# Optimization experiments

Hardware: AMD Instinct MI355X
Metric: run time of the kernel (lower is better)

Reference implementation:

```python
import jax, jax.numpy as jnp
import numpy as np

RES_SCALE = 0.1
B, C, H, W = 16, 256, 96, 96


def conv3x3(x, w):
    # NCHW input, OIHW weight, SAME padding (padding=1 for k=3), no bias
    return jax.lax.conv_general_dilated(
        x, w, window_strides=(1, 1), padding="SAME",
        dimension_numbers=("NCHW", "OIHW", "NCHW"))


def setup_inputs() -> dict:
    key = jax.random.key(0)
    k1, k2, k3, k4 = jax.random.split(key, 4)
    fan = C * 9
    x = jax.random.normal(k1, (B, C, H, W), dtype=jnp.float32)
    conv2_w = jax.random.normal(k2, (C, C, 3, 3), dtype=jnp.float32) / np.sqrt(fan)
    conv3_w = jax.random.normal(k3, (C, C, 3, 3), dtype=jnp.float32) / np.sqrt(fan)
    prelu_w = jnp.full((1,), 0.25, dtype=jnp.float32)  # nn.PReLU default init
    # interleaved channel partition: P=0::3 (86), R=1::3 (85), T=2::3 (85)
    idx_p = jnp.arange(0, C, 3, dtype=jnp.int32)
    idx_r = jnp.arange(1, C, 3, dtype=jnp.int32)
    idx_t = jnp.arange(2, C, 3, dtype=jnp.int32)
    return {"x": x, "conv2_w": conv2_w, "conv3_w": conv3_w, "prelu_w": prelu_w,
            "idx_p": idx_p, "idx_r": idx_r, "idx_t": idx_t}


def reference(x, conv2_w, conv3_w, prelu_w, idx_p, idx_r, idx_t):
    # op2 = conv2(prune(x, skip_gate)) ; all-ones gate -> identity prune
    op2 = conv3x3(x, conv2_w)  # [B, C, H, W]
    # per-channel activation routing (gathers permute channel order to [P,R,T])
    gp = op2[:, idx_p]                                  # [B, 86, H, W]
    a = jnp.concatenate([
        jnp.where(gp >= 0, gp, prelu_w[0] * gp),        # PReLU (1 shared param)
        jax.nn.relu(op2[:, idx_r]),                     # [B, 85, H, W]
        jnp.tanh(op2[:, idx_t]),                        # [B, 85, H, W]
    ], axis=1)                                          # [B, C, H, W]
    # conv_tot branch: op3 = conv3(a)*res_scale + x * reshape(skip_conv_gate)
    # skip_conv_gate == ones here, so the skip scaling is identity
    op3 = conv3x3(a, conv3_w) * RES_SCALE + x
    return op3


if __name__ == "__main__":
    out = reference(**setup_inputs())
    print(out.shape, out.dtype)
```

## Files before the change

### kernel.cpp

```cpp
#include <hip/hip_runtime.h>
#include <math.h>


#define Bn 16
#define Cn 256
#define Hn 96
#define Wn 96
#define PH 98
#define PW 98
#define HW (Hn*Wn)

typedef __bf16 bf16x8 __attribute__((ext_vector_type(8)));
typedef float  f32x4  __attribute__((ext_vector_type(4)));

__device__ __forceinline__ unsigned short f2bf(float f) {
    unsigned int u = __float_as_uint(f);
    unsigned int r = (u + 0x7fffu + ((u >> 16) & 1u)) >> 16;
    return (unsigned short)r;
}

__device__ __forceinline__ void lds_load16(void* lds, const void* g) {
    auto gp = (const __attribute__((address_space(1))) char*)(unsigned long long)(uintptr_t)g;
    auto lp = (__attribute__((address_space(3))) char*)(unsigned int)(uintptr_t)lds;
    __builtin_amdgcn_global_load_lds(gp, lp, 16, 0, 0);
}

#define SB() __builtin_amdgcn_sched_barrier(0)
#define MEMFENCE() asm volatile("" ::: "memory")

__global__ __launch_bounds__(256)
void zero_border_k(unsigned short* __restrict__ t) {
    int idx = blockIdx.x * 256 + threadIdx.x;
    int oct = idx & 31;
    int rest = idx >> 5;
    int pidx = rest % 388;
    int b = rest / 388;
    int h, w;
    if (pidx < 98)       { h = 0;  w = pidx; }
    else if (pidx < 196) { h = 97; w = pidx - 98; }
    else if (pidx < 292) { h = pidx - 196 + 1; w = 0; }
    else                 { h = pidx - 292 + 1; w = 97; }
    size_t e = ((size_t)(b * PH + h) * PW + w) * 256 + oct * 8;
    *(uint4*)(t + e) = make_uint4(0u, 0u, 0u, 0u);
}

template<bool PERM>
__global__ __launch_bounds__(256)
void pack_w_k(const float* __restrict__ w, unsigned short* __restrict__ wp) {
    int idx = blockIdx.x * 256 + threadIdx.x;
    int ci_l = idx & 31;
    int c    = (idx >> 5) & 255;
    int v    = idx >> 13;
    int k9   = v % 9;
    int cc   = v / 9;
    int co;
    if (PERM) {
        co = (c < 86) ? c * 3 : (c < 171) ? (c - 86) * 3 + 1 : (c - 171) * 3 + 2;
    } else {
        co = c;
    }
    float val = w[((size_t)co * 256 + cc * 32 + ci_l) * 9 + k9];
    wp[idx] = f2bf(val);
}

__global__ __launch_bounds__(256)
void transform_x_k(const float* __restrict__ x, unsigned short* __restrict__ xp) {
    __shared__ float s[32 * 33];
    const int t = threadIdx.x;
    const int col0 = blockIdx.x * 32;
    const int row  = blockIdx.y;
    const int z = blockIdx.z;
    const int b = z >> 3;
    const int ci0 = (z & 7) * 32;

    #pragma unroll
    for (int i = 0; i < 4; ++i) {
        int ci = i * 8 + (t >> 5);
        int px = t & 31;
        s[ci * 33 + px] = x[((size_t)(b * Cn + ci0 + ci)) * HW + row * Wn + col0 + px];
    }
    __syncthreads();
    const int px = t >> 3;
    const int c4 = (t & 7) * 4;
    ushort4 o;
    o.x = f2bf(s[(c4 + 0) * 33 + px]);
    o.y = f2bf(s[(c4 + 1) * 33 + px]);
    o.z = f2bf(s[(c4 + 2) * 33 + px]);
    o.w = f2bf(s[(c4 + 3) * 33 + px]);
    size_t e = ((size_t)(b * PH + row + 1) * PW + (col0 + px + 1)) * 256 + ci0 + c4;
    *(ushort4*)(xp + e) = o;
}

template<int MODE>
__global__ __launch_bounds__(512) __attribute__((amdgpu_waves_per_eu(2, 2)))
void conv_k(const unsigned short* __restrict__ in_cl,
            const unsigned short* __restrict__ wp,
            const float* __restrict__ prelu_w,
            const float* __restrict__ xres,
            void* __restrict__ outp)
{
    __shared__ unsigned short s_x[2][2048 * 8];
    __shared__ unsigned short s_w[2][1536 * 8];

    const int tid = threadIdx.x;
    const int bid = blockIdx.x;
    const int wg = (bid & 7) * 96 + (bid >> 3);
    const int blk_co = (wg & 1) * 128;
    const int t2 = wg >> 1;
    const int tile = t2 % 24;
    const int b = t2 / 24;
    const int R0 = (tile / 3) * 12;
    const int C0 = (tile % 3) * 32;

    const int lane = tid & 63;
    const int wv = tid >> 6;
    const int l15 = lane & 15;
    const int qq = lane >> 4;
    const int cg = wv & 1;
    const int wrow = wv >> 1;
    const int qa = qq ^ ((l15 >> 1) & 3);

    const unsigned short* img = in_cl + (size_t)b * PH * PW * 256;

    int xg[4];
    #pragma unroll
    for (int i = 0; i < 4; ++i) {
        int slot = i * 512 + tid;
        int lsl = slot ^ ((slot >> 3) & 3);
        if (lsl > 1903) lsl = 1903;
        int p = lsl >> 2;
        int pr = p / 34, pc = p - pr * 34;
        xg[i] = ((R0 + pr) * PW + (C0 + pc)) * 256 + (lsl & 3) * 8;
    }
    int wbase[3];
    #pragma unroll
    for (int i = 0; i < 3; ++i) {
        int slot = i * 512 + tid;
        int lsl = slot ^ ((slot >> 3) & 3);
        int kw = lsl >> 9;
        int co = (lsl >> 2) & 127;
        wbase[i] = kw * 8192 + (blk_co + co) * 32 + (lsl & 3) * 8;
    }

    f32x4 acc[4][6];
    #pragma unroll
    for (int m = 0; m < 4; ++m)
        #pragma unroll
        for (int n = 0; n < 6; ++n) acc[m][n] = 0.f;

    #pragma unroll
    for (int i = 0; i < 3; ++i) lds_load16(&s_w[0][(size_t)(i * 512 + tid) * 8], wp + wbase[i]);
    #pragma unroll
    for (int i = 0; i < 4; ++i) lds_load16(&s_x[0][(size_t)(i * 512 + tid) * 8], img + xg[i]);
    MEMFENCE(); SB();
    asm volatile("s_waitcnt vmcnt(0)" ::: "memory");
    SB();
    __builtin_amdgcn_s_barrier();
    SB();

#define LOADW(AF, KW) {                                                           \
    _Pragma("unroll")                                                             \
    for (int m = 0; m < 4; ++m) {                                                 \
        const int row_ = (KW) * 128 + cg * 64 + m * 16 + l15;                     \
        AF[m] = *(const bf16x8*)&swc[row_ * 32 + qa * 8];                         \
    }                                                                             \
}
#define LOADX(BF, KW) {                                                           \
    _Pragma("unroll")                                                             \
    for (int n = 0; n < 6; ++n) {                                                 \
        const int P_ = (wrow * 3 + (n >> 1) + kh) * 34 + (n & 1) * 16 + l15 + (KW); \
        BF[n] = *(const bf16x8*)&sxc[P_ * 32 + ((qq ^ ((P_ >> 1) & 3)) << 3)];    \
    }                                                                             \
}
#define MFMA_ON(AF, BF) {                                                         \
    __builtin_amdgcn_s_setprio(1);                                                \
    _Pragma("unroll")                                                             \
    for (int n = 0; n < 6; ++n)                                                   \
        _Pragma("unroll")                                                         \
        for (int m = 0; m < 4; ++m)                                               \
            acc[m][n] = __builtin_amdgcn_mfma_f32_16x16x32_bf16(AF[m], BF[n], acc[m][n], 0, 0, 0); \
    __builtin_amdgcn_s_setprio(0);                                                \
}

    for (int s = 0; s < 24; ++s) {
        const int c  = s / 3;
        const int kh = s - 3 * c;
        const unsigned short* swc = s_w[s & 1];
        const unsigned short* sxc = s_x[c & 1];
        const bool stage_x = (kh == 1) && (c < 7);

        if (s < 23) {
            #pragma unroll
            for (int i = 0; i < 3; ++i)
                lds_load16(&s_w[(s + 1) & 1][(size_t)(i * 512 + tid) * 8],
                           wp + (size_t)(s + 1) * 24576 + wbase[i]);
            MEMFENCE(); SB();
        }
        if (stage_x) {
            #pragma unroll
            for (int i = 0; i < 4; ++i)
                lds_load16(&s_x[(c + 1) & 1][(size_t)(i * 512 + tid) * 8],
                           img + xg[i] + (c + 1) * 32);
            MEMFENCE(); SB();
        }

        {
            bf16x8 afA[4], bfA[6], afB[4], bfB[6];
            LOADW(afA, 0); LOADX(bfA, 0);
            LOADW(afB, 1); LOADX(bfB, 1);
            MFMA_ON(afA, bfA);
            LOADW(afA, 2); LOADX(bfA, 2);
            MFMA_ON(afB, bfB);
            MFMA_ON(afA, bfA);
        }

        if (stage_x) {
            asm volatile("s_waitcnt vmcnt(4)" ::: "memory");
        } else {
            asm volatile("s_waitcnt vmcnt(0)" ::: "memory");
        }
        SB();
        __builtin_amdgcn_s_barrier();
        SB();
    }
#undef LOADW
#undef LOADX
#undef MFMA_ON

    if constexpr (MODE == 0) {
        const float pw = prelu_w[0];
        unsigned short* aout = (unsigned short*)outp;
        #pragma unroll
        for (int n = 0; n < 6; ++n) {
            const int row_p = wrow * 3 + (n >> 1);
            const int col_p = (n & 1) * 16 + l15;
            size_t pix = ((size_t)(b * PH + R0 + row_p + 1)) * PW + (C0 + col_p + 1);
            #pragma unroll
            for (int m = 0; m < 4; ++m) {
                const int cb = blk_co + cg * 64 + m * 16 + qq * 4;
                float r[4];
                #pragma unroll
                for (int j = 0; j < 4; ++j) {
                    const int ch = cb + j;
                    float s = acc[m][n][j];
                    if (ch < 86)        r[j] = s >= 0.f ? s : pw * s;
                    else if (ch < 171)  r[j] = fmaxf(s, 0.f);
                    else {
                        float e = __expf(2.f * s);
                        r[j] = 1.f - 2.f / (e + 1.f);
                    }
                }
                ushort4 o;
                o.x = f2bf(r[0]); o.y = f2bf(r[1]); o.z = f2bf(r[2]); o.w = f2bf(r[3]);
                *(ushort4*)(aout + pix * 256 + cb) = o;
            }
        }
    } else {
        float* fout = (float*)outp;
        #pragma unroll
        for (int n = 0; n < 6; ++n) {
            const int row_p = wrow * 3 + (n >> 1);
            const int col_p = (n & 1) * 16 + l15;
            #pragma unroll
            for (int m = 0; m < 4; ++m) {
                const int cb = blk_co + cg * 64 + m * 16 + qq * 4;
                size_t base = ((size_t)(b * Cn + cb)) * HW + (size_t)(R0 + row_p) * Wn + (C0 + col_p);
                #pragma unroll
                for (int j = 0; j < 4; ++j)
                    fout[base + (size_t)j * HW] = acc[m][n][j] * 0.1f + xres[base + (size_t)j * HW];
            }
        }
    }
}

extern "C" void kernel_launch(void* const* d_in, const int* in_sizes, int n_in,
                              void* d_out, int out_size, void* d_ws, size_t ws_size,
                              hipStream_t stream) {
    const float* x  = (const float*)d_in[0];
    const float* w2 = (const float*)d_in[1];
    const float* w3 = (const float*)d_in[2];
    const float* pw = (const float*)d_in[3];
    float* out = (float*)d_out;
    char* ws = (char*)d_ws;

    unsigned short* a_cl = (unsigned short*)ws;
    unsigned short* wp2  = (unsigned short*)(ws + 78675968);
    unsigned short* wp3  = (unsigned short*)(ws + 78675968 + 1179648);
    unsigned short* x_pad = (unsigned short*)d_out;

    zero_border_k<<<776, 256, 0, stream>>>(x_pad);
    zero_border_k<<<776, 256, 0, stream>>>(a_cl);
    pack_w_k<true ><<<2304, 256, 0, stream>>>(w2, wp2);
    pack_w_k<false><<<2304, 256, 0, stream>>>(w3, wp3);
    transform_x_k<<<dim3(3, 96, 128), 256, 0, stream>>>(x, x_pad);

    conv_k<0><<<768, 512, 0, stream>>>(x_pad, wp2, pw, nullptr, (void*)a_cl);
    conv_k<1><<<768, 512, 0, stream>>>(a_cl, wp3, nullptr, x, (void*)out);
}
```

Baseline: 405.6 us.

## Interleave global-to-LDS staging with per-kw LDS reads and MFMA phases

Restructures the inner conv loop so each of the three kw sub-steps issues its LDS fragment reads, then one slice of the next-stage weight/input global_load_lds, then a barrier and its MFMA block. Global prefetches are spread across the kw phases instead of issued in bursts at the top of each stage. This adds two barriers per kw phase (six per stage instead of one) and drops the double-register A/B fragment overlap. The aim is a more even load/compute interleave, at the cost of more synchronisation.

After: 438.5 us. 8.1% more time.

```diff
diff --git a/kernel.cpp b/kernel.cpp
--- a/kernel.cpp
+++ b/kernel.cpp
@@ -158,74 +158,58 @@
     __builtin_amdgcn_s_barrier();
     SB();
 
-#define LOADW(AF, KW) {                                                           \
-    _Pragma("unroll")                                                             \
-    for (int m = 0; m < 4; ++m) {                                                 \
-        const int row_ = (KW) * 128 + cg * 64 + m * 16 + l15;                     \
-        AF[m] = *(const bf16x8*)&swc[row_ * 32 + qa * 8];                         \
-    }                                                                             \
-}
-#define LOADX(BF, KW) {                                                           \
-    _Pragma("unroll")                                                             \
-    for (int n = 0; n < 6; ++n) {                                                 \
-        const int P_ = (wrow * 3 + (n >> 1) + kh) * 34 + (n & 1) * 16 + l15 + (KW); \
-        BF[n] = *(const bf16x8*)&sxc[P_ * 32 + ((qq ^ ((P_ >> 1) & 3)) << 3)];    \
-    }                                                                             \
-}
-#define MFMA_ON(AF, BF) {                                                         \
-    __builtin_amdgcn_s_setprio(1);                                                \
-    _Pragma("unroll")                                                             \
-    for (int n = 0; n < 6; ++n)                                                   \
-        _Pragma("unroll")                                                         \
-        for (int m = 0; m < 4; ++m)                                               \
-            acc[m][n] = __builtin_amdgcn_mfma_f32_16x16x32_bf16(AF[m], BF[n], acc[m][n], 0, 0, 0); \
-    __builtin_amdgcn_s_setprio(0);                                                \
-}
-
     for (int s = 0; s < 24; ++s) {
         const int c  = s / 3;
         const int kh = s - 3 * c;
         const unsigned short* swc = s_w[s & 1];
         const unsigned short* sxc = s_x[c & 1];
-        const bool stage_x = (kh == 1) && (c < 7);
-
-        if (s < 23) {
-            #pragma unroll
-            for (int i = 0; i < 3; ++i)
-                lds_load16(&s_w[(s + 1) & 1][(size_t)(i * 512 + tid) * 8],
-                           wp + (size_t)(s + 1) * 24576 + wbase[i]);
+
+        #pragma unroll
+        for (int kw = 0; kw < 3; ++kw) {
+            bf16x8 af[4], bf[6];
+            #pragma unroll
+            for (int m = 0; m < 4; ++m) {
+                const int row_ = kw * 128 + cg * 64 + m * 16 + l15;
+                af[m] = *(const bf16x8*)&swc[row_ * 32 + qa * 8];
+            }
+            #pragma unroll
+            for (int n = 0; n < 6; ++n) {
+                const int P_ = (wrow * 3 + (n >> 1) + kh) * 34 + (n & 1) * 16 + l15 + kw;
+                bf[n] = *(const bf16x8*)&sxc[P_ * 32 + ((qq ^ ((P_ >> 1) & 3)) << 3)];
+            }
+            if (s < 23)
+                lds_load16(&s_w[(s + 1) & 1][(size_t)(kw * 512 + tid) * 8],
+                           wp + (size_t)(s + 1) * 24576 + wbase[kw]);
+            if (c < 7) {
+                if (kh == 1)
+                    lds_load16(&s_x[(c + 1) & 1][(size_t)(kw * 512 + tid) * 8],
+                               img + xg[kw] + (c + 1) * 32);
+                else if (kh == 2 && kw == 0)
+                    lds_load16(&s_x[(c + 1) & 1][(size_t)(3 * 512 + tid) * 8],
+                               img + xg[3] + (c + 1) * 32);
+            }
             MEMFENCE(); SB();
+            __builtin_amdgcn_s_barrier();
+            asm volatile("s_waitcnt lgkmcnt(0)" ::: "memory");
+            SB();
+            __builtin_amdgcn_s_setprio(1);
+            #pragma unroll
+            for (int n = 0; n < 6; ++n)
+                #pragma unroll
+                for (int m = 0; m < 4; ++m)
+                    acc[m][n] = __builtin_amdgcn_mfma_f32_16x16x32_bf16(af[m], bf[n], acc[m][n], 0, 0, 0);
+            __builtin_amdgcn_s_setprio(0);
+            SB();
+            if (kw == 2) {
+                if (kh == 1 && c < 7)
+                    asm volatile("s_waitcnt vmcnt(1)" ::: "memory");
+                else
+                    asm volatile("s_waitcnt vmcnt(0)" ::: "memory");
+                SB();
+            }
+            __builtin_amdgcn_s_barrier();
         }
-        if (stage_x) {
-            #pragma unroll
-            for (int i = 0; i < 4; ++i)
-                lds_load16(&s_x[(c + 1) & 1][(size_t)(i * 512 + tid) * 8],
-                           img + xg[i] + (c + 1) * 32);
-            MEMFENCE(); SB();
-        }
-
-        {
-            bf16x8 afA[4], bfA[6], afB[4], bfB[6];
-            LOADW(afA, 0); LOADX(bfA, 0);
-            LOADW(afB, 1); LOADX(bfB, 1);
-            MFMA_ON(afA, bfA);
-            LOADW(afA, 2); LOADX(bfA, 2);
-            MFMA_ON(afB, bfB);
-            MFMA_ON(afA, bfA);
-        }
-
-        if (stage_x) {
-            asm volatile("s_waitcnt vmcnt(4)" ::: "memory");
-        } else {
-            asm volatile("s_waitcnt vmcnt(0)" ::: "memory");
-        }
-        SB();
-        __builtin_amdgcn_s_barrier();
-        SB();
-    }
-#undef LOADW
-#undef LOADX
-#undef MFMA_ON
+    }
 
     if constexpr (MODE == 0) {
         const float pw = prelu_w[0];
```

## Triple-buffer weight stages and spread input prefetch across kh substeps

Applied to the files above, without the earlier changes.

Weights move from double to triple LDS buffering with a prefetch distance of two stages. The channel loop is unrolled into three kh substeps, and the next input-channel block load is split between the first two substeps. Explicit lgkmcnt waits let MFMAs start while later LDS fragment reads are still in flight, and vmcnt drains are tuned per substep so each barrier waits on less global traffic. This raises LDS usage and makes the hand-counted waitcnt values fragile.

Result: slower. 1.296 ms (+219.4%).

```diff
diff --git a/kernel.cpp b/kernel.cpp
--- a/kernel.cpp
+++ b/kernel.cpp
@@ -100,7 +100,7 @@
             void* __restrict__ outp)
 {
     __shared__ unsigned short s_x[2][2048 * 8];
-    __shared__ unsigned short s_w[2][1536 * 8];
+    __shared__ unsigned short s_w[3][1536 * 8];
 
     const int tid = threadIdx.x;
     const int bid = blockIdx.x;
@@ -151,6 +151,8 @@
     #pragma unroll
     for (int i = 0; i < 3; ++i) lds_load16(&s_w[0][(size_t)(i * 512 + tid) * 8], wp + wbase[i]);
     #pragma unroll
+    for (int i = 0; i < 3; ++i) lds_load16(&s_w[1][(size_t)(i * 512 + tid) * 8], wp + 24576 + wbase[i]);
+    #pragma unroll
     for (int i = 0; i < 4; ++i) lds_load16(&s_x[0][(size_t)(i * 512 + tid) * 8], img + xg[i]);
     MEMFENCE(); SB();
     asm volatile("s_waitcnt vmcnt(0)" ::: "memory");
@@ -158,73 +160,72 @@
     __builtin_amdgcn_s_barrier();
     SB();
 
-#define LOADW(AF, KW) {                                                           \
+#define LOADF(AF, BF, KH, KW) {                                                   \
     _Pragma("unroll")                                                             \
     for (int m = 0; m < 4; ++m) {                                                 \
         const int row_ = (KW) * 128 + cg * 64 + m * 16 + l15;                     \
         AF[m] = *(const bf16x8*)&swc[row_ * 32 + qa * 8];                         \
     }                                                                             \
-}
-#define LOADX(BF, KW) {                                                           \
     _Pragma("unroll")                                                             \
     for (int n = 0; n < 6; ++n) {                                                 \
-        const int P_ = (wrow * 3 + (n >> 1) + kh) * 34 + (n & 1) * 16 + l15 + (KW); \
+        const int P_ = (wrow * 3 + (n >> 1) + (KH)) * 34 + (n & 1) * 16 + l15 + (KW); \
         BF[n] = *(const bf16x8*)&sxc[P_ * 32 + ((qq ^ ((P_ >> 1) & 3)) << 3)];    \
     }                                                                             \
 }
 #define MFMA_ON(AF, BF) {                                                         \
-    __builtin_amdgcn_s_setprio(1);                                                \
     _Pragma("unroll")                                                             \
     for (int n = 0; n < 6; ++n)                                                   \
         _Pragma("unroll")                                                         \
         for (int m = 0; m < 4; ++m)                                               \
             acc[m][n] = __builtin_amdgcn_mfma_f32_16x16x32_bf16(AF[m], BF[n], acc[m][n], 0, 0, 0); \
+}
+
+#define SUBSTEP(KH, WST, WGI, DOW, NX, VDRAIN_MAIN, VDRAIN_TAIL) {                \
+    const unsigned short* swc = s_w[(KH)];                                        \
+    const unsigned short* sxc = s_x[c & 1];                                       \
+    bf16x8 a0[4], b0[6], a1[4], b1[6], a2[4], b2[6];                              \
+    LOADF(a0, b0, KH, 0);                                                         \
+    LOADF(a1, b1, KH, 1);                                                         \
+    if (DOW) {                                                                    \
+        _Pragma("unroll")                                                         \
+        for (int i = 0; i < 3; ++i)                                               \
+            lds_load16(&s_w[(WST)][(size_t)(i * 512 + tid) * 8],                  \
+                       wp + (size_t)(WGI) * 24576 + wbase[i]);                    \
+    }                                                                             \
+    if ((NX) == 3 && c < 7) {                                                     \
+        _Pragma("unroll")                                                         \
+        for (int i = 0; i < 3; ++i)                                               \
+            lds_load16(&s_x[(c + 1) & 1][(size_t)(i * 512 + tid) * 8],            \
+                       img + xg[i] + (c + 1) * 32);                               \
+    }                                                                             \
+    if ((NX) == 1 && c < 7)                                                       \
+        lds_load16(&s_x[(c + 1) & 1][(size_t)(3 * 512 + tid) * 8],                \
+                   img + xg[3] + (c + 1) * 32);                                   \
+    MEMFENCE(); SB();                                                             \
+    __builtin_amdgcn_s_setprio(1);                                                \
+    asm volatile("s_waitcnt lgkmcnt(10)" ::: "memory"); SB();                     \
+    MFMA_ON(a0, b0);                                                              \
+    LOADF(a2, b2, KH, 2);                                                         \
+    MEMFENCE(); SB();                                                             \
+    asm volatile("s_waitcnt lgkmcnt(10)" ::: "memory"); SB();                     \
+    MFMA_ON(a1, b1);                                                              \
+    asm volatile("s_waitcnt lgkmcnt(0)" ::: "memory"); SB();                      \
+    MFMA_ON(a2, b2);                                                              \
     __builtin_amdgcn_s_setprio(0);                                                \
-}
-
-    for (int s = 0; s < 24; ++s) {
-        const int c  = s / 3;
-        const int kh = s - 3 * c;
-        const unsigned short* swc = s_w[s & 1];
-        const unsigned short* sxc = s_x[c & 1];
-        const bool stage_x = (kh == 1) && (c < 7);
-
-        if (s < 23) {
-            #pragma unroll
-            for (int i = 0; i < 3; ++i)
-                lds_load16(&s_w[(s + 1) & 1][(size_t)(i * 512 + tid) * 8],
-                           wp + (size_t)(s + 1) * 24576 + wbase[i]);
-            MEMFENCE(); SB();
-        }
-        if (stage_x) {
-            #pragma unroll
-            for (int i = 0; i < 4; ++i)
-                lds_load16(&s_x[(c + 1) & 1][(size_t)(i * 512 + tid) * 8],
-                           img + xg[i] + (c + 1) * 32);
-            MEMFENCE(); SB();
-        }
-
-        {
-            bf16x8 afA[4], bfA[6], afB[4], bfB[6];
-            LOADW(afA, 0); LOADX(bfA, 0);
-            LOADW(afB, 1); LOADX(bfB, 1);
-            MFMA_ON(afA, bfA);
-            LOADW(afA, 2); LOADX(bfA, 2);
-            MFMA_ON(afB, bfB);
-            MFMA_ON(afA, bfA);
-        }
-
-        if (stage_x) {
-            asm volatile("s_waitcnt vmcnt(4)" ::: "memory");
-        } else {
-            asm volatile("s_waitcnt vmcnt(0)" ::: "memory");
-        }
-        SB();
-        __builtin_amdgcn_s_barrier();
-        SB();
-    }
-#undef LOADW
-#undef LOADX
+    if (c < 7) { asm volatile("s_waitcnt vmcnt(" #VDRAIN_MAIN ")" ::: "memory"); }\
+    else       { asm volatile("s_waitcnt vmcnt(" #VDRAIN_TAIL ")" ::: "memory"); }\
+    SB();                                                                         \
+    __builtin_amdgcn_s_barrier();                                                 \
+    SB();                                                                         \
+}
+
+    for (int c = 0; c < 8; ++c) {
+        SUBSTEP(0, 2, (3 * c + 2), true,      3, 6, 3)
+        SUBSTEP(1, 0, (3 * c + 3), (c < 7),   1, 7, 0)
+        SUBSTEP(2, 1, (3 * c + 4), (c < 7),   0, 3, 0)
+    }
+#undef SUBSTEP
+#undef LOADF
 #undef MFMA_ON
 
     if constexpr (MODE == 0) {
```
